# Performance work log

Hardware: AMD Instinct MI355X
Metric: run time of the kernel (lower is better)

## Reference

```python
import jax, jax.numpy as jnp
import numpy as np

B, N, C, H = 2, 2048, 768, 12
D = C // H
HID = 4 * C  # 3072
EPS = 1e-5
PAD = 128  # last PAD key positions are padded


def _layer_norm(x, w, b):
    m = jnp.mean(x, axis=-1, keepdims=True)
    v = jnp.var(x, axis=-1, keepdims=True)
    return (x - m) * jax.lax.rsqrt(v + EPS) * w + b


def setup_inputs() -> dict:
    key = jax.random.key(0)
    ks = jax.random.split(key, 12)
    s = 0.02
    inp = {
        'x': jax.random.normal(ks[0], (B, N, C), jnp.float32),
        # keys at positions >= N-PAD are padded (mask must have some True to be exercised)
        'padding_mask': jnp.broadcast_to(jnp.arange(N) >= N - PAD, (B, N)),
        'alibi_bias': jax.random.normal(ks[1], (B, H, N, N), jnp.float32) * 0.1,
        'qkv_w': jax.random.normal(ks[2], (3 * C, C), jnp.float32) * s,
        'qkv_b': jnp.zeros((3 * C,), jnp.float32),
        'proj_w': jax.random.normal(ks[3], (C, C), jnp.float32) * s,
        'proj_b': jnp.zeros((C,), jnp.float32),
        'norm1_w': jnp.ones((C,), jnp.float32),
        'norm1_b': jnp.zeros((C,), jnp.float32),
        'norm2_w': jnp.ones((C,), jnp.float32),
        'norm2_b': jnp.zeros((C,), jnp.float32),
        'fc1_w': jax.random.normal(ks[4], (HID, C), jnp.float32) * s,
        'fc1_b': jnp.zeros((HID,), jnp.float32),
        'fc2_w': jax.random.normal(ks[5], (C, HID), jnp.float32) * s,
        'fc2_b': jnp.zeros((C,), jnp.float32),
    }
    return inp


def _attention(x, padding_mask, alibi_bias, qkv_w, qkv_b, proj_w, proj_b):
    scale = D ** (-0.5)
    qkv = (x @ qkv_w.T + qkv_b).reshape(B, N, 3, H, D).transpose(2, 0, 3, 1, 4)
    q, k, v = qkv[0] * scale, qkv[1], qkv[2]  # [B,H,N,D]
    attn = jnp.einsum('bhnd,bhmd->bhnm', q, k)
    attn = attn + alibi_bias  # alibi covers all heads here
    attn = jnp.where(padding_mask[:, None, None, :], -jnp.inf, attn)
    attn = jax.nn.softmax(attn.astype(jnp.float32), axis=-1).astype(x.dtype)
    out = jnp.einsum('bhnm,bhmd->bhnd', attn, v)
    out = out.transpose(0, 2, 1, 3).reshape(B, N, C)
    return out @ proj_w.T + proj_b


def _mlp(x, fc1_w, fc1_b, fc2_w, fc2_b):
    h = jax.nn.gelu(x @ fc1_w.T + fc1_b, approximate=False)
    return h @ fc2_w.T + fc2_b


def reference(x, padding_mask, alibi_bias, qkv_w, qkv_b, proj_w, proj_b,
              norm1_w, norm1_b, norm2_w, norm2_b, fc1_w, fc1_b, fc2_w, fc2_b):
    # layer_norm_first=True, eval mode (dropouts/drop_path = identity)
    h = x + _attention(_layer_norm(x, norm1_w, norm1_b), padding_mask, alibi_bias,
                       qkv_w, qkv_b, proj_w, proj_b)
    # Faithful to source quirk: `r = x = self.mlp(self.norm2(x))` drops the residual,
    # so output = mlp_out + mlp_out and t = mlp_out.
    t = _mlp(_layer_norm(h, norm2_w, norm2_b), fc1_w, fc1_b, fc2_w, fc2_b)
    return (t + t, t)
```

## Files before the change

### kernel.cpp

```cpp
#include <hip/hip_runtime.h>
#include <cstdint>
#include <cstddef>

#define B_   2
#define N_   2048
#define C_   768
#define H_   12
#define D_   64
#define HID_ 3072
#define BH_  24
#define MM   4096

typedef __attribute__((ext_vector_type(8))) short s16x8;
typedef __attribute__((ext_vector_type(4))) short s16x4;
typedef __attribute__((ext_vector_type(4))) float f32x4;

__device__ __forceinline__ short f2bf(float f) {
  uint32_t u = __float_as_uint(f);
  u += 0x7fffu + ((u >> 16) & 1u);
  return (short)(u >> 16);
}

__device__ __forceinline__ void gl_lds16(const void* g, void* l) {
  __builtin_amdgcn_global_load_lds((const __attribute__((address_space(1))) void*)g,
                                   (__attribute__((address_space(3))) void*)l,
                                   16, 0, 0);
}

__device__ __forceinline__ float gelu_tanh(float v) {
  const float z  = 0.7978845608f * v * (1.0f + 0.044715f * v * v);
  const float e  = __expf(-2.0f * fabsf(z));
  const float th = copysignf((1.0f - e) / (1.0f + e), z);
  return 0.5f * v * (1.0f + th);
}

__global__ __launch_bounds__(256) void k_cvt4(
    const float* __restrict__ a, short* __restrict__ oa,
    const float* __restrict__ b, short* __restrict__ ob,
    const float* __restrict__ c, short* __restrict__ oc,
    const float* __restrict__ d, short* __restrict__ od) {
  const int blk = blockIdx.x;
  const float* in; short* out; int base;
  if (blk < 1728)      { in = a; out = oa; base = blk; }
  else if (blk < 2304) { in = b; out = ob; base = blk - 1728; }
  else if (blk < 4608) { in = c; out = oc; base = blk - 2304; }
  else                 { in = d; out = od; base = blk - 4608; }
  const int i = (base * 256 + threadIdx.x) * 4;
  float4 v = *(const float4*)(in + i);
  s16x4 o;
  o[0] = f2bf(v.x); o[1] = f2bf(v.y); o[2] = f2bf(v.z); o[3] = f2bf(v.w);
  *(s16x4*)(out + i) = o;
}

__global__ __launch_bounds__(256) void k_ln(const float* __restrict__ x,
                                            const float* __restrict__ w,
                                            const float* __restrict__ b,
                                            short* __restrict__ out) {
  const int row = blockIdx.x, t = threadIdx.x;
  const float* xr = x + (size_t)row * C_;
  float a0 = xr[t], a1 = xr[t + 256], a2 = xr[t + 512];
  float s = a0 + a1 + a2;
  float q = a0 * a0 + a1 * a1 + a2 * a2;
  #pragma unroll
  for (int off = 32; off >= 1; off >>= 1) {
    s += __shfl_xor(s, off);
    q += __shfl_xor(q, off);
  }
  __shared__ float ps[4], pq[4];
  if ((t & 63) == 0) { ps[t >> 6] = s; pq[t >> 6] = q; }
  __syncthreads();
  s = ps[0] + ps[1] + ps[2] + ps[3];
  q = pq[0] + pq[1] + pq[2] + pq[3];
  const float mean = s * (1.0f / C_);
  const float var  = q * (1.0f / C_) - mean * mean;
  const float rs   = rsqrtf(var + 1e-5f);
  short* orow = out + (size_t)row * C_;
  orow[t]       = f2bf((a0 - mean) * rs * w[t]       + b[t]);
  orow[t + 256] = f2bf((a1 - mean) * rs * w[t + 256] + b[t + 256]);
  orow[t + 512] = f2bf((a2 - mean) * rs * w[t + 512] + b[t + 512]);
}

__device__ __forceinline__ void gemm_core(const short* __restrict__ A,
                                          const short* __restrict__ Bw,
                                          int ldk, int kbeg, int kend,
                                          short* As, short* Bs,
                                          f32x4 acc[4][4]) {
  const int tid = threadIdx.x, lane = tid & 63, wid = tid >> 6;
  const int wm = wid & 1, wn = wid >> 1;
  const int l15 = lane & 15, quad = lane >> 4;
  const size_t bm = (size_t)blockIdx.x * 128, bn = (size_t)blockIdx.y * 128;
  #pragma unroll
  for (int mi = 0; mi < 4; ++mi)
    #pragma unroll
    for (int ni = 0; ni < 4; ++ni)
      acc[mi][ni] = (f32x4){0.f, 0.f, 0.f, 0.f};
  const int rrow = lane >> 2;
  const int rcol = (lane & 3) * 8;
  for (int k0 = kbeg; k0 < kend; k0 += 32) {
    #pragma unroll
    for (int i = 0; i < 2; ++i) {
      const int rg = wid * 2 + i;
      gl_lds16(A  + (bm + rg * 16 + rrow) * (size_t)ldk + k0 + rcol, As + rg * 512);
      gl_lds16(Bw + (bn + rg * 16 + rrow) * (size_t)ldk + k0 + rcol, Bs + rg * 512);
    }
    __syncthreads();
    s16x8 af[4], bf[4];
    #pragma unroll
    for (int mi = 0; mi < 4; ++mi)
      af[mi] = *(const s16x8*)(As + (wm * 64 + mi * 16 + l15) * 32 + quad * 8);
    #pragma unroll
    for (int ni = 0; ni < 4; ++ni)
      bf[ni] = *(const s16x8*)(Bs + (wn * 64 + ni * 16 + l15) * 32 + quad * 8);
    #pragma unroll
    for (int mi = 0; mi < 4; ++mi)
      #pragma unroll
      for (int ni = 0; ni < 4; ++ni)
        acc[mi][ni] = __builtin_amdgcn_mfma_f32_16x16x32_bf16(af[mi], bf[ni],
                                                              acc[mi][ni], 0, 0, 0);
    __syncthreads();
  }
}

__global__ __launch_bounds__(256) void k_gemm_qkv(const short* __restrict__ A,
    const short* __restrict__ W, const float* __restrict__ bias,
    short* __restrict__ qb, short* __restrict__ kb, short* __restrict__ vb) {
  __shared__ short As[4096], Bs[4096];
  f32x4 acc[4][4];
  gemm_core(A, W, C_, 0, C_, As, Bs, acc);
  const int lane = threadIdx.x & 63, wid = threadIdx.x >> 6;
  const int wm = wid & 1, wn = wid >> 1, quad = lane >> 4, l15 = lane & 15;
  const int m0 = blockIdx.x * 128 + wm * 64;
  const int n0 = blockIdx.y * 128 + wn * 64;
  #pragma unroll
  for (int ni = 0; ni < 4; ++ni) {
    const int n = n0 + ni * 16 + l15;
    const int s = n / C_, rem = n % C_;
    const int h = rem >> 6, d = rem & 63;
    short* dst = (s == 0) ? qb : (s == 1) ? kb : vb;
    const float scale = (s == 0) ? 0.125f : 1.0f;
    const float bv = bias[n];
    #pragma unroll
    for (int mi = 0; mi < 4; ++mi)
      #pragma unroll
      for (int r = 0; r < 4; ++r) {
        const int m = m0 + mi * 16 + quad * 4 + r;
        const int bb = m >> 11, pos = m & 2047;
        dst[(((size_t)bb * H_ + h) * N_ + pos) * D_ + d] =
            f2bf((acc[mi][ni][r] + bv) * scale);
      }
  }
}

__global__ __launch_bounds__(256) void k_trans_v(const short* __restrict__ v,
                                                 short* __restrict__ vt) {
  __shared__ short t[64][68];
  const int bh = blockIdx.y;
  const int p0 = blockIdx.x * 64;
  #pragma unroll
  for (int i = 0; i < 16; ++i) {
    const int idx = threadIdx.x + i * 256;
    const int r = idx >> 6, c = idx & 63;
    t[r][c] = v[((size_t)bh * N_ + p0 + r) * D_ + c];
  }
  __syncthreads();
  #pragma unroll
  for (int i = 0; i < 16; ++i) {
    const int idx = threadIdx.x + i * 256;
    const int r = idx >> 6, c = idx & 63;
    vt[((size_t)bh * D_ + r) * N_ + p0 + c] = t[c][r];
  }
}

__global__ __launch_bounds__(256) void k_attn(const short* __restrict__ qb,
    const short* __restrict__ kb, const short* __restrict__ vtb,
    const float* __restrict__ alibi, const int* __restrict__ mask,
    short* __restrict__ aout) {
  __shared__ short Ks[64 * 72], Vs[64 * 72];
  const int tid = threadIdx.x, lane = tid & 63, wid = tid >> 6;
  const int quad = lane >> 4, l15 = lane & 15;
  const int bh = blockIdx.y, bb = bh / H_, hh = bh % H_;
  const int qg = blockIdx.x * 64 + wid * 16 + l15;

  const short* qrow = qb + ((size_t)bh * N_ + qg) * D_;
  const s16x8 qf0 = *(const s16x8*)(qrow + quad * 8);
  const s16x8 qf1 = *(const s16x8*)(qrow + 32 + quad * 8);

  f32x4 oacc[4];
  #pragma unroll
  for (int i = 0; i < 4; ++i) oacc[i] = (f32x4){0.f, 0.f, 0.f, 0.f};
  float mrun = -1e30f, lrun = 0.f;

  const float* arow = alibi + ((size_t)bh * N_ + qg) * N_;
  const int* mrow = mask + bb * N_;

  for (int jt = 0; jt < N_; jt += 64) {
    int4 mk[4];
    int anyvalid = 0;
    #pragma unroll
    for (int ji = 0; ji < 4; ++ji) {
      mk[ji] = *(const int4*)(mrow + jt + ji * 16 + quad * 4);
      if (!(mk[ji].x && mk[ji].y && mk[ji].z && mk[ji].w)) anyvalid = 1;
    }
    if (!__any(anyvalid)) continue;

    #pragma unroll
    for (int c = 0; c < 2; ++c) {
      const int idx = tid + c * 256;
      const int row = idx >> 3, col = (idx & 7) * 8;
      *(int4*)(&Ks[row * 72 + col]) =
          *(const int4*)(kb + ((size_t)bh * N_ + jt + row) * D_ + col);
      *(int4*)(&Vs[row * 72 + col]) =
          *(const int4*)(vtb + ((size_t)bh * D_ + row) * N_ + jt + col);
    }
    __syncthreads();

    f32x4 s[4];
    #pragma unroll
    for (int ji = 0; ji < 4; ++ji) {
      const s16x8 ka = *(const s16x8*)(&Ks[(ji * 16 + l15) * 72 + quad * 8]);
      const s16x8 kc = *(const s16x8*)(&Ks[(ji * 16 + l15) * 72 + 32 + quad * 8]);
      f32x4 z = (f32x4){0.f, 0.f, 0.f, 0.f};
      z = __builtin_amdgcn_mfma_f32_16x16x32_bf16(ka, qf0, z, 0, 0, 0);
      s[ji] = __builtin_amdgcn_mfma_f32_16x16x32_bf16(kc, qf1, z, 0, 0, 0);
    }

    float p[4][4];
    float mt = -1e30f;
    #pragma unroll
    for (int ji = 0; ji < 4; ++ji) {
      const float4 al = *(const float4*)(arow + jt + ji * 16 + quad * 4);
      float v0 = s[ji][0] + al.x; if (mk[ji].x) v0 = -1e30f;
      float v1 = s[ji][1] + al.y; if (mk[ji].y) v1 = -1e30f;
      float v2 = s[ji][2] + al.z; if (mk[ji].z) v2 = -1e30f;
      float v3 = s[ji][3] + al.w; if (mk[ji].w) v3 = -1e30f;
      p[ji][0] = v0; p[ji][1] = v1; p[ji][2] = v2; p[ji][3] = v3;
      mt = fmaxf(mt, fmaxf(fmaxf(v0, v1), fmaxf(v2, v3)));
    }
    mt = fmaxf(mt, __shfl_xor(mt, 16));
    mt = fmaxf(mt, __shfl_xor(mt, 32));
    const float mnew = fmaxf(mrun, mt);
    const float scl = __expf(mrun - mnew);
    float psum = 0.f;
    s16x4 pf[4];
    #pragma unroll
    for (int ji = 0; ji < 4; ++ji)
      #pragma unroll
      for (int r = 0; r < 4; ++r) {
        const float e = __expf(p[ji][r] - mnew);
        psum += e;
        pf[ji][r] = f2bf(e);
      }
    psum += __shfl_xor(psum, 16);
    psum += __shfl_xor(psum, 32);
    lrun = lrun * scl + psum;
    mrun = mnew;
    #pragma unroll
    for (int i = 0; i < 4; ++i) oacc[i] *= scl;

    #pragma unroll
    for (int ji = 0; ji < 4; ++ji)
      #pragma unroll
      for (int ni = 0; ni < 4; ++ni) {
        const s16x4 vf = *(const s16x4*)(&Vs[(ni * 16 + l15) * 72 + ji * 16 + quad * 4]);
        oacc[ni] = __builtin_amdgcn_mfma_f32_16x16x16bf16_1k(vf, pf[ji],
                                                             oacc[ni], 0, 0, 0);
      }
    __syncthreads();
  }

  const float inv = 1.0f / lrun;
  short* orow = aout + ((size_t)bb * N_ + qg) * C_ + hh * D_;
  #pragma unroll
  for (int ni = 0; ni < 4; ++ni)
    #pragma unroll
    for (int r = 0; r < 4; ++r)
      orow[ni * 16 + quad * 4 + r] = f2bf(oacc[ni][r] * inv);
}

__global__ __launch_bounds__(256) void k_gemm_projs(const short* __restrict__ A,
    const short* __restrict__ W, float* __restrict__ part) {
  __shared__ short As[4096], Bs[4096];
  f32x4 acc[4][4];
  const int z = blockIdx.z;
  gemm_core(A, W, C_, z * 384, z * 384 + 384, As, Bs, acc);
  const int lane = threadIdx.x & 63, wid = threadIdx.x >> 6;
  const int wm = wid & 1, wn = wid >> 1, quad = lane >> 4, l15 = lane & 15;
  const int m0 = blockIdx.x * 128 + wm * 64;
  const int n0 = blockIdx.y * 128 + wn * 64;
  float* pz = part + (size_t)z * MM * C_;
  #pragma unroll
  for (int ni = 0; ni < 4; ++ni) {
    const int n = n0 + ni * 16 + l15;
    #pragma unroll
    for (int mi = 0; mi < 4; ++mi)
      #pragma unroll
      for (int r = 0; r < 4; ++r) {
        const int m = m0 + mi * 16 + quad * 4 + r;
        pz[(size_t)m * C_ + n] = acc[mi][ni][r];
      }
  }
}

__global__ __launch_bounds__(256) void k_proj_red(const float* __restrict__ p,
    const float* __restrict__ bias, const float* __restrict__ xres,
    float* __restrict__ hout) {
  const int i = (blockIdx.x * 256 + threadIdx.x) * 4;
  const float4 s0 = *(const float4*)(p + i);
  const float4 s1 = *(const float4*)(p + (size_t)MM * C_ + i);
  const float4 bv = *(const float4*)(bias + (i % C_));
  const float4 xr = *(const float4*)(xres + i);
  float4 o;
  o.x = s0.x + s1.x + bv.x + xr.x;
  o.y = s0.y + s1.y + bv.y + xr.y;
  o.z = s0.z + s1.z + bv.z + xr.z;
  o.w = s0.w + s1.w + bv.w + xr.w;
  *(float4*)(hout + i) = o;
}

__global__ __launch_bounds__(256) void k_gemm_fc1(const short* __restrict__ A,
    const short* __restrict__ W, const float* __restrict__ bias,
    short* __restrict__ hid) {
  __shared__ short As[4096], Bs[4096];
  f32x4 acc[4][4];
  gemm_core(A, W, C_, 0, C_, As, Bs, acc);
  const int lane = threadIdx.x & 63, wid = threadIdx.x >> 6;
  const int wm = wid & 1, wn = wid >> 1, quad = lane >> 4, l15 = lane & 15;
  const int m0 = blockIdx.x * 128 + wm * 64;
  const int n0 = blockIdx.y * 128 + wn * 64;
  #pragma unroll
  for (int ni = 0; ni < 4; ++ni) {
    const int n = n0 + ni * 16 + l15;
    const float bv = bias[n];
    #pragma unroll
    for (int mi = 0; mi < 4; ++mi)
      #pragma unroll
      for (int r = 0; r < 4; ++r) {
        const int m = m0 + mi * 16 + quad * 4 + r;
        hid[(size_t)m * HID_ + n] = f2bf(gelu_tanh(acc[mi][ni][r] + bv));
      }
  }
}

__global__ __launch_bounds__(256) void k_gemm_fc2s(const short* __restrict__ A,
    const short* __restrict__ W, float* __restrict__ part) {
  __shared__ short As[4096], Bs[4096];
  f32x4 acc[4][4];
  const int z = blockIdx.z;
  gemm_core(A, W, HID_, z * 768, z * 768 + 768, As, Bs, acc);
  const int lane = threadIdx.x & 63, wid = threadIdx.x >> 6;
  const int wm = wid & 1, wn = wid >> 1, quad = lane >> 4, l15 = lane & 15;
  const int m0 = blockIdx.x * 128 + wm * 64;
  const int n0 = blockIdx.y * 128 + wn * 64;
  float* pz = part + (size_t)z * MM * C_;
  #pragma unroll
  for (int ni = 0; ni < 4; ++ni) {
    const int n = n0 + ni * 16 + l15;
    #pragma unroll
    for (int mi = 0; mi < 4; ++mi)
      #pragma unroll
      for (int r = 0; r < 4; ++r) {
        const int m = m0 + mi * 16 + quad * 4 + r;
        pz[(size_t)m * C_ + n] = acc[mi][ni][r];
      }
  }
}

__global__ __launch_bounds__(256) void k_fc2_red(const float* __restrict__ p,
    const float* __restrict__ bias, float* __restrict__ out) {
  const int i = (blockIdx.x * 256 + threadIdx.x) * 4;
  const float4 s0 = *(const float4*)(p + i);
  const float4 s1 = *(const float4*)(p + (size_t)MM * C_ + i);
  const float4 s2 = *(const float4*)(p + (size_t)2 * MM * C_ + i);
  const float4 s3 = *(const float4*)(p + (size_t)3 * MM * C_ + i);
  const float4 bv = *(const float4*)(bias + (i % C_));
  float4 t, t2;
  t.x = s0.x + s1.x + s2.x + s3.x + bv.x;  t2.x = t.x + t.x;
  t.y = s0.y + s1.y + s2.y + s3.y + bv.y;  t2.y = t.y + t.y;
  t.z = s0.z + s1.z + s2.z + s3.z + bv.z;  t2.z = t.z + t.z;
  t.w = s0.w + s1.w + s2.w + s3.w + bv.w;  t2.w = t.w + t.w;
  *(float4*)(out + i) = t2;
  *(float4*)(out + (size_t)MM * C_ + i) = t;
}

extern "C" void kernel_launch(void* const* d_in, const int* in_sizes, int n_in,
                              void* d_out, int out_size, void* d_ws, size_t ws_size,
                              hipStream_t stream) {
  (void)in_sizes; (void)n_in; (void)out_size; (void)ws_size;
  const float* x      = (const float*)d_in[0];
  const int*   mask   = (const int*)  d_in[1];
  const float* alibi  = (const float*)d_in[2];
  const float* qkv_w  = (const float*)d_in[3];
  const float* qkv_b  = (const float*)d_in[4];
  const float* proj_w = (const float*)d_in[5];
  const float* proj_b = (const float*)d_in[6];
  const float* n1w    = (const float*)d_in[7];
  const float* n1b    = (const float*)d_in[8];
  const float* n2w    = (const float*)d_in[9];
  const float* n2b    = (const float*)d_in[10];
  const float* fc1_w  = (const float*)d_in[11];
  const float* fc1_b  = (const float*)d_in[12];
  const float* fc2_w  = (const float*)d_in[13];
  const float* fc2_b  = (const float*)d_in[14];
  float* out = (float*)d_out;

  char* ws = (char*)d_ws;
  size_t off = 0;
  auto alloc = [&](size_t bytes) -> void* {
    void* p = ws + off;
    off += (bytes + 255) & ~(size_t)255;
    return p;
  };
  short* wq   = (short*)alloc((size_t)3 * C_ * C_ * 2);
  short* wp   = (short*)alloc((size_t)C_ * C_ * 2);
  short* wf1  = (short*)alloc((size_t)HID_ * C_ * 2);
  short* wf2  = (short*)alloc((size_t)C_ * HID_ * 2);
  short* xln  = (short*)alloc((size_t)MM * C_ * 2);
  short* qb   = (short*)alloc((size_t)BH_ * N_ * D_ * 2);
  short* kb   = (short*)alloc((size_t)BH_ * N_ * D_ * 2);
  short* vb   = (short*)alloc((size_t)BH_ * N_ * D_ * 2);
  short* vtb  = (short*)alloc((size_t)BH_ * D_ * N_ * 2);
  float* h    = (float*)alloc((size_t)MM * C_ * 4);
  short* hid  = (short*)alloc((size_t)MM * HID_ * 2);
  float* ppj  = (float*)alloc((size_t)2 * MM * C_ * 4);
  float* pf2  = (float*)alloc((size_t)4 * MM * C_ * 4);
  short* hln  = xln;
  short* aout = vb;

  k_cvt4<<<6912, 256, 0, stream>>>(qkv_w, wq, proj_w, wp, fc1_w, wf1, fc2_w, wf2);

  k_ln<<<MM, 256, 0, stream>>>(x, n1w, n1b, xln);
  k_gemm_qkv<<<dim3(MM / 128, 3 * C_ / 128), 256, 0, stream>>>(xln, wq, qkv_b,
                                                               qb, kb, vb);
  k_trans_v<<<dim3(N_ / 64, BH_), 256, 0, stream>>>(vb, vtb);
  k_attn<<<dim3(N_ / 64, BH_), 256, 0, stream>>>(qb, kb, vtb, alibi, mask, aout);
  k_gemm_projs<<<dim3(MM / 128, C_ / 128, 2), 256, 0, stream>>>(aout, wp, ppj);
  k_proj_red<<<MM * C_ / 1024, 256, 0, stream>>>(ppj, proj_b, x, h);
  k_ln<<<MM, 256, 0, stream>>>(h, n2w, n2b, hln);
  k_gemm_fc1<<<dim3(MM / 128, HID_ / 128), 256, 0, stream>>>(hln, wf1, fc1_b, hid);
  k_gemm_fc2s<<<dim3(MM / 128, C_ / 128, 4), 256, 0, stream>>>(hid, wf2, pf2);
  k_fc2_red<<<MM * C_ / 1024, 256, 0, stream>>>(pf2, fc2_b, out);
}
```

Measured before the change: 749.4 us.

## Fuse LN with weight casts, fuse proj reduction into LN2, widen GEMM/attention tiles

Merges the weight bf16 conversion and first layernorm into one launch, and folds the projection split-K reduction and residual add into the second layernorm so the fp32 h buffer is never written. The shared GEMM core now stages a K-step of 64 per barrier instead of 32, halving the synchronisations. Attention processes 128-key tiles loaded through direct global-to-LDS copies, with the padding mask precomputed once per block as an additive LDS vector and per-tile skip flags. This trades extra LDS per block, which may lower occupancy, for fewer launches, fewer barriers and less memory traffic.

```diff
diff --git a/kernel.cpp b/kernel.cpp
--- a/kernel.cpp
+++ b/kernel.cpp
@@ -34,50 +34,50 @@
   return 0.5f * v * (1.0f + th);
 }
 
-__global__ __launch_bounds__(256) void k_cvt4(
+__global__ __launch_bounds__(256) void k_pre(const float* __restrict__ x,
+    const float* __restrict__ n1w, const float* __restrict__ n1b,
+    short* __restrict__ xln,
     const float* __restrict__ a, short* __restrict__ oa,
     const float* __restrict__ b, short* __restrict__ ob,
     const float* __restrict__ c, short* __restrict__ oc,
     const float* __restrict__ d, short* __restrict__ od) {
-  const int blk = blockIdx.x;
-  const float* in; short* out; int base;
-  if (blk < 1728)      { in = a; out = oa; base = blk; }
-  else if (blk < 2304) { in = b; out = ob; base = blk - 1728; }
-  else if (blk < 4608) { in = c; out = oc; base = blk - 2304; }
-  else                 { in = d; out = od; base = blk - 4608; }
-  const int i = (base * 256 + threadIdx.x) * 4;
-  float4 v = *(const float4*)(in + i);
-  s16x4 o;
-  o[0] = f2bf(v.x); o[1] = f2bf(v.y); o[2] = f2bf(v.z); o[3] = f2bf(v.w);
-  *(s16x4*)(out + i) = o;
-}
-
-__global__ __launch_bounds__(256) void k_ln(const float* __restrict__ x,
-                                            const float* __restrict__ w,
-                                            const float* __restrict__ b,
-                                            short* __restrict__ out) {
-  const int row = blockIdx.x, t = threadIdx.x;
-  const float* xr = x + (size_t)row * C_;
-  float a0 = xr[t], a1 = xr[t + 256], a2 = xr[t + 512];
-  float s = a0 + a1 + a2;
-  float q = a0 * a0 + a1 * a1 + a2 * a2;
-  #pragma unroll
-  for (int off = 32; off >= 1; off >>= 1) {
-    s += __shfl_xor(s, off);
-    q += __shfl_xor(q, off);
-  }
-  __shared__ float ps[4], pq[4];
-  if ((t & 63) == 0) { ps[t >> 6] = s; pq[t >> 6] = q; }
-  __syncthreads();
-  s = ps[0] + ps[1] + ps[2] + ps[3];
-  q = pq[0] + pq[1] + pq[2] + pq[3];
-  const float mean = s * (1.0f / C_);
-  const float var  = q * (1.0f / C_) - mean * mean;
-  const float rs   = rsqrtf(var + 1e-5f);
-  short* orow = out + (size_t)row * C_;
-  orow[t]       = f2bf((a0 - mean) * rs * w[t]       + b[t]);
-  orow[t + 256] = f2bf((a1 - mean) * rs * w[t + 256] + b[t + 256]);
-  orow[t + 512] = f2bf((a2 - mean) * rs * w[t + 512] + b[t + 512]);
+  const int t = threadIdx.x;
+  if (blockIdx.x < MM) {
+    const int row = blockIdx.x;
+    const float* xr = x + (size_t)row * C_;
+    float a0 = xr[t], a1 = xr[t + 256], a2 = xr[t + 512];
+    float s = a0 + a1 + a2;
+    float q = a0 * a0 + a1 * a1 + a2 * a2;
+    #pragma unroll
+    for (int off = 32; off >= 1; off >>= 1) {
+      s += __shfl_xor(s, off);
+      q += __shfl_xor(q, off);
+    }
+    __shared__ float ps[4], pq[4];
+    if ((t & 63) == 0) { ps[t >> 6] = s; pq[t >> 6] = q; }
+    __syncthreads();
+    s = ps[0] + ps[1] + ps[2] + ps[3];
+    q = pq[0] + pq[1] + pq[2] + pq[3];
+    const float mean = s * (1.0f / C_);
+    const float var  = q * (1.0f / C_) - mean * mean;
+    const float rs   = rsqrtf(var + 1e-5f);
+    short* orow = xln + (size_t)row * C_;
+    orow[t]       = f2bf((a0 - mean) * rs * n1w[t]       + n1b[t]);
+    orow[t + 256] = f2bf((a1 - mean) * rs * n1w[t + 256] + n1b[t + 256]);
+    orow[t + 512] = f2bf((a2 - mean) * rs * n1w[t + 512] + n1b[t + 512]);
+  } else {
+    const int blk = blockIdx.x - MM;
+    const float* in; short* out; int base;
+    if (blk < 1728)      { in = a; out = oa; base = blk; }
+    else if (blk < 2304) { in = b; out = ob; base = blk - 1728; }
+    else if (blk < 4608) { in = c; out = oc; base = blk - 2304; }
+    else                 { in = d; out = od; base = blk - 4608; }
+    const int i = (base * 256 + t) * 4;
+    float4 v = *(const float4*)(in + i);
+    s16x4 o;
+    o[0] = f2bf(v.x); o[1] = f2bf(v.y); o[2] = f2bf(v.z); o[3] = f2bf(v.w);
+    *(s16x4*)(out + i) = o;
+  }
 }
 
 __device__ __forceinline__ void gemm_core(const short* __restrict__ A,
@@ -94,29 +94,36 @@
     #pragma unroll
     for (int ni = 0; ni < 4; ++ni)
       acc[mi][ni] = (f32x4){0.f, 0.f, 0.f, 0.f};
-  const int rrow = lane >> 2;
-  const int rcol = (lane & 3) * 8;
-  for (int k0 = kbeg; k0 < kend; k0 += 32) {
-    #pragma unroll
-    for (int i = 0; i < 2; ++i) {
-      const int rg = wid * 2 + i;
-      gl_lds16(A  + (bm + rg * 16 + rrow) * (size_t)ldk + k0 + rcol, As + rg * 512);
-      gl_lds16(Bw + (bn + rg * 16 + rrow) * (size_t)ldk + k0 + rcol, Bs + rg * 512);
-    }
+  const int r4 = lane >> 2;
+  const int c4 = lane & 3;
+  for (int k0 = kbeg; k0 < kend; k0 += 64) {
+    #pragma unroll
+    for (int p = 0; p < 2; ++p)
+      #pragma unroll
+      for (int c = 0; c < 2; ++c) {
+        const int g = c * 4 + wid;
+        gl_lds16(A  + (bm + g * 16 + r4) * (size_t)ldk + k0 + p * 32 + c4 * 8,
+                 As + p * 4096 + g * 512);
+        gl_lds16(Bw + (bn + g * 16 + r4) * (size_t)ldk + k0 + p * 32 + c4 * 8,
+                 Bs + p * 4096 + g * 512);
+      }
     __syncthreads();
-    s16x8 af[4], bf[4];
-    #pragma unroll
-    for (int mi = 0; mi < 4; ++mi)
-      af[mi] = *(const s16x8*)(As + (wm * 64 + mi * 16 + l15) * 32 + quad * 8);
-    #pragma unroll
-    for (int ni = 0; ni < 4; ++ni)
-      bf[ni] = *(const s16x8*)(Bs + (wn * 64 + ni * 16 + l15) * 32 + quad * 8);
-    #pragma unroll
-    for (int mi = 0; mi < 4; ++mi)
+    #pragma unroll
+    for (int h = 0; h < 2; ++h) {
+      s16x8 af[4], bf[4];
+      #pragma unroll
+      for (int mi = 0; mi < 4; ++mi)
+        af[mi] = *(const s16x8*)(As + h * 4096 + (wm * 64 + mi * 16 + l15) * 32 + quad * 8);
       #pragma unroll
       for (int ni = 0; ni < 4; ++ni)
-        acc[mi][ni] = __builtin_amdgcn_mfma_f32_16x16x32_bf16(af[mi], bf[ni],
-                                                              acc[mi][ni], 0, 0, 0);
+        bf[ni] = *(const s16x8*)(Bs + h * 4096 + (wn * 64 + ni * 16 + l15) * 32 + quad * 8);
+      #pragma unroll
+      for (int mi = 0; mi < 4; ++mi)
+        #pragma unroll
+        for (int ni = 0; ni < 4; ++ni)
+          acc[mi][ni] = __builtin_amdgcn_mfma_f32_16x16x32_bf16(af[mi], bf[ni],
+                                                                acc[mi][ni], 0, 0, 0);
+    }
     __syncthreads();
   }
 }
@@ -124,7 +131,7 @@
 __global__ __launch_bounds__(256) void k_gemm_qkv(const short* __restrict__ A,
     const short* __restrict__ W, const float* __restrict__ bias,
     short* __restrict__ qb, short* __restrict__ kb, short* __restrict__ vb) {
-  __shared__ short As[4096], Bs[4096];
+  __shared__ short As[8192], Bs[8192];
   f32x4 acc[4][4];
   gemm_core(A, W, C_, 0, C_, As, Bs, acc);
   const int lane = threadIdx.x & 63, wid = threadIdx.x >> 6;
@@ -175,11 +182,29 @@
     const short* __restrict__ kb, const short* __restrict__ vtb,
     const float* __restrict__ alibi, const int* __restrict__ mask,
     short* __restrict__ aout) {
-  __shared__ short Ks[64 * 72], Vs[64 * 72];
+  __shared__ short Ks[8192];
+  __shared__ short Vs[8192];
+  __shared__ float Madd[N_];
+  __shared__ int   Tflag[16];
   const int tid = threadIdx.x, lane = tid & 63, wid = tid >> 6;
   const int quad = lane >> 4, l15 = lane & 15;
+  const int r4 = lane >> 2, c4 = lane & 3;
   const int bh = blockIdx.y, bb = bh / H_, hh = bh % H_;
   const int qg = blockIdx.x * 64 + wid * 16 + l15;
+
+  if (tid < 16) Tflag[tid] = 0;
+  __syncthreads();
+  {
+    const int j0 = tid * 8;
+    int anyv = 0;
+    #pragma unroll
+    for (int i = 0; i < 8; ++i) {
+      const int mv = mask[bb * N_ + j0 + i];
+      Madd[j0 + i] = mv ? -1e30f : 0.0f;
+      anyv |= (mv == 0);
+    }
+    if (anyv) atomicOr(&Tflag[j0 >> 7], 1);
+  }
 
   const short* qrow = qb + ((size_t)bh * N_ + qg) * D_;
   const s16x8 qf0 = *(const s16x8*)(qrow + quad * 8);
@@ -189,51 +214,47 @@
   #pragma unroll
   for (int i = 0; i < 4; ++i) oacc[i] = (f32x4){0.f, 0.f, 0.f, 0.f};
   float mrun = -1e30f, lrun = 0.f;
-
   const float* arow = alibi + ((size_t)bh * N_ + qg) * N_;
-  const int* mrow = mask + bb * N_;
-
-  for (int jt = 0; jt < N_; jt += 64) {
-    int4 mk[4];
-    int anyvalid = 0;
-    #pragma unroll
-    for (int ji = 0; ji < 4; ++ji) {
-      mk[ji] = *(const int4*)(mrow + jt + ji * 16 + quad * 4);
-      if (!(mk[ji].x && mk[ji].y && mk[ji].z && mk[ji].w)) anyvalid = 1;
-    }
-    if (!__any(anyvalid)) continue;
-
-    #pragma unroll
-    for (int c = 0; c < 2; ++c) {
-      const int idx = tid + c * 256;
-      const int row = idx >> 3, col = (idx & 7) * 8;
-      *(int4*)(&Ks[row * 72 + col]) =
-          *(const int4*)(kb + ((size_t)bh * N_ + jt + row) * D_ + col);
-      *(int4*)(&Vs[row * 72 + col]) =
-          *(const int4*)(vtb + ((size_t)bh * D_ + row) * N_ + jt + col);
-    }
+  __syncthreads();
+
+  for (int t = 0; t < 16; ++t) {
+    if (!Tflag[t]) continue;
+    const int jt = t * 128;
+    #pragma unroll
+    for (int p = 0; p < 2; ++p)
+      #pragma unroll
+      for (int c = 0; c < 2; ++c) {
+        const int g = c * 4 + wid;
+        gl_lds16(kb + ((size_t)bh * N_ + jt + g * 16 + r4) * D_ + p * 32 + c4 * 8,
+                 Ks + p * 4096 + g * 512);
+      }
+    #pragma unroll
+    for (int p = 0; p < 4; ++p)
+      gl_lds16(vtb + ((size_t)bh * D_ + wid * 16 + r4) * N_ + jt + p * 32 + c4 * 8,
+               Vs + p * 2048 + wid * 512);
     __syncthreads();
 
-    f32x4 s[4];
-    #pragma unroll
-    for (int ji = 0; ji < 4; ++ji) {
-      const s16x8 ka = *(const s16x8*)(&Ks[(ji * 16 + l15) * 72 + quad * 8]);
-      const s16x8 kc = *(const s16x8*)(&Ks[(ji * 16 + l15) * 72 + 32 + quad * 8]);
+    f32x4 s[8];
+    #pragma unroll
+    for (int ji = 0; ji < 8; ++ji) {
+      const s16x8 ka = *(const s16x8*)(Ks + (ji * 16 + l15) * 32 + quad * 8);
+      const s16x8 kc = *(const s16x8*)(Ks + 4096 + (ji * 16 + l15) * 32 + quad * 8);
       f32x4 z = (f32x4){0.f, 0.f, 0.f, 0.f};
       z = __builtin_amdgcn_mfma_f32_16x16x32_bf16(ka, qf0, z, 0, 0, 0);
       s[ji] = __builtin_amdgcn_mfma_f32_16x16x32_bf16(kc, qf1, z, 0, 0, 0);
     }
 
-    float p[4][4];
+    float p_[8][4];
     float mt = -1e30f;
     #pragma unroll
-    for (int ji = 0; ji < 4; ++ji) {
+    for (int ji = 0; ji < 8; ++ji) {
       const float4 al = *(const float4*)(arow + jt + ji * 16 + quad * 4);
-      float v0 = s[ji][0] + al.x; if (mk[ji].x) v0 = -1e30f;
-      float v1 = s[ji][1] + al.y; if (mk[ji].y) v1 = -1e30f;
-      float v2 = s[ji][2] + al.z; if (mk[ji].z) v2 = -1e30f;
-      float v3 = s[ji][3] + al.w; if (mk[ji].w) v3 = -1e30f;
-      p[ji][0] = v0; p[ji][1] = v1; p[ji][2] = v2; p[ji][3] = v3;
+      const float4 md = *(const float4*)(&Madd[jt + ji * 16 + quad * 4]);
+      const float v0 = s[ji][0] + al.x + md.x;
+      const float v1 = s[ji][1] + al.y + md.y;
+      const float v2 = s[ji][2] + al.z + md.z;
+      const float v3 = s[ji][3] + al.w + md.w;
+      p_[ji][0] = v0; p_[ji][1] = v1; p_[ji][2] = v2; p_[ji][3] = v3;
       mt = fmaxf(mt, fmaxf(fmaxf(v0, v1), fmaxf(v2, v3)));
     }
     mt = fmaxf(mt, __shfl_xor(mt, 16));
@@ -241,12 +262,12 @@
     const float mnew = fmaxf(mrun, mt);
     const float scl = __expf(mrun - mnew);
     float psum = 0.f;
-    s16x4 pf[4];
-    #pragma unroll
-    for (int ji = 0; ji < 4; ++ji)
+    s16x4 pf[8];
+    #pragma unroll
+    for (int ji = 0; ji < 8; ++ji)
       #pragma unroll
       for (int r = 0; r < 4; ++r) {
-        const float e = __expf(p[ji][r] - mnew);
+        const float e = __expf(p_[ji][r] - mnew);
         psum += e;
         pf[ji][r] = f2bf(e);
       }
@@ -258,13 +279,15 @@
     for (int i = 0; i < 4; ++i) oacc[i] *= scl;
 
     #pragma unroll
-    for (int ji = 0; ji < 4; ++ji)
+    for (int jj = 0; jj < 8; ++jj) {
+      const int pnl = jj >> 1, jw = (jj & 1) * 16 + quad * 4;
       #pragma unroll
       for (int ni = 0; ni < 4; ++ni) {
-        const s16x4 vf = *(const s16x4*)(&Vs[(ni * 16 + l15) * 72 + ji * 16 + quad * 4]);
-        oacc[ni] = __builtin_amdgcn_mfma_f32_16x16x16bf16_1k(vf, pf[ji],
+        const s16x4 vf = *(const s16x4*)(Vs + pnl * 2048 + (ni * 16 + l15) * 32 + jw);
+        oacc[ni] = __builtin_amdgcn_mfma_f32_16x16x16bf16_1k(vf, pf[jj],
                                                              oacc[ni], 0, 0, 0);
       }
+    }
     __syncthreads();
   }
 
@@ -279,7 +302,7 @@
 
 __global__ __launch_bounds__(256) void k_gemm_projs(const short* __restrict__ A,
     const short* __restrict__ W, float* __restrict__ part) {
-  __shared__ short As[4096], Bs[4096];
+  __shared__ short As[8192], Bs[8192];
   f32x4 acc[4][4];
   const int z = blockIdx.z;
   gemm_core(A, W, C_, z * 384, z * 384 + 384, As, Bs, acc);
@@ -301,26 +324,43 @@
   }
 }
 
-__global__ __launch_bounds__(256) void k_proj_red(const float* __restrict__ p,
+__global__ __launch_bounds__(256) void k_ln2p(const float* __restrict__ p,
     const float* __restrict__ bias, const float* __restrict__ xres,
-    float* __restrict__ hout) {
-  const int i = (blockIdx.x * 256 + threadIdx.x) * 4;
-  const float4 s0 = *(const float4*)(p + i);
-  const float4 s1 = *(const float4*)(p + (size_t)MM * C_ + i);
-  const float4 bv = *(const float4*)(bias + (i % C_));
-  const float4 xr = *(const float4*)(xres + i);
-  float4 o;
-  o.x = s0.x + s1.x + bv.x + xr.x;
-  o.y = s0.y + s1.y + bv.y + xr.y;
-  o.z = s0.z + s1.z + bv.z + xr.z;
-  o.w = s0.w + s1.w + bv.w + xr.w;
-  *(float4*)(hout + i) = o;
+    const float* __restrict__ w, const float* __restrict__ b,
+    short* __restrict__ out) {
+  const int row = blockIdx.x, t = threadIdx.x;
+  const size_t base = (size_t)row * C_;
+  float a0 = p[base + t]       + p[(size_t)MM * C_ + base + t]
+           + bias[t]           + xres[base + t];
+  float a1 = p[base + t + 256] + p[(size_t)MM * C_ + base + t + 256]
+           + bias[t + 256]     + xres[base + t + 256];
+  float a2 = p[base + t + 512] + p[(size_t)MM * C_ + base + t + 512]
+           + bias[t + 512]     + xres[base + t + 512];
+  float s = a0 + a1 + a2;
+  float q = a0 * a0 + a1 * a1 + a2 * a2;
+  #pragma unroll
+  for (int off = 32; off >= 1; off >>= 1) {
+    s += __shfl_xor(s, off);
+    q += __shfl_xor(q, off);
+  }
+  __shared__ float ps[4], pq[4];
+  if ((t & 63) == 0) { ps[t >> 6] = s; pq[t >> 6] = q; }
+  __syncthreads();
+  s = ps[0] + ps[1] + ps[2] + ps[3];
+  q = pq[0] + pq[1] + pq[2] + pq[3];
+  const float mean = s * (1.0f / C_);
+  const float var  = q * (1.0f / C_) - mean * mean;
+  const float rs   = rsqrtf(var + 1e-5f);
+  short* orow = out + base;
+  orow[t]       = f2bf((a0 - mean) * rs * w[t]       + b[t]);
+  orow[t + 256] = f2bf((a1 - mean) * rs * w[t + 256] + b[t + 256]);
+  orow[t + 512] = f2bf((a2 - mean) * rs * w[t + 512] + b[t + 512]);
 }
 
 __global__ __launch_bounds__(256) void k_gemm_fc1(const short* __restrict__ A,
     const short* __restrict__ W, const float* __restrict__ bias,
     short* __restrict__ hid) {
-  __shared__ short As[4096], Bs[4096];
+  __shared__ short As[8192], Bs[8192];
   f32x4 acc[4][4];
   gemm_core(A, W, C_, 0, C_, As, Bs, acc);
   const int lane = threadIdx.x & 63, wid = threadIdx.x >> 6;
@@ -343,7 +383,7 @@
 
 __global__ __launch_bounds__(256) void k_gemm_fc2s(const short* __restrict__ A,
     const short* __restrict__ W, float* __restrict__ part) {
-  __shared__ short As[4096], Bs[4096];
+  __shared__ short As[8192], Bs[8192];
   f32x4 acc[4][4];
   const int z = blockIdx.z;
   gemm_core(A, W, HID_, z * 768, z * 768 + 768, As, Bs, acc);
@@ -419,23 +459,21 @@
   short* kb   = (short*)alloc((size_t)BH_ * N_ * D_ * 2);
   short* vb   = (short*)alloc((size_t)BH_ * N_ * D_ * 2);
   short* vtb  = (short*)alloc((size_t)BH_ * D_ * N_ * 2);
-  float* h    = (float*)alloc((size_t)MM * C_ * 4);
   short* hid  = (short*)alloc((size_t)MM * HID_ * 2);
   float* ppj  = (float*)alloc((size_t)2 * MM * C_ * 4);
   float* pf2  = (float*)alloc((size_t)4 * MM * C_ * 4);
   short* hln  = xln;
   short* aout = vb;
 
-  k_cvt4<<<6912, 256, 0, stream>>>(qkv_w, wq, proj_w, wp, fc1_w, wf1, fc2_w, wf2);
-
-  k_ln<<<MM, 256, 0, stream>>>(x, n1w, n1b, xln);
+  k_pre<<<MM + 6912, 256, 0, stream>>>(x, n1w, n1b, xln,
+                                       qkv_w, wq, proj_w, wp,
+                                       fc1_w, wf1, fc2_w, wf2);
   k_gemm_qkv<<<dim3(MM / 128, 3 * C_ / 128), 256, 0, stream>>>(xln, wq, qkv_b,
                                                                qb, kb, vb);
   k_trans_v<<<dim3(N_ / 64, BH_), 256, 0, stream>>>(vb, vtb);
   k_attn<<<dim3(N_ / 64, BH_), 256, 0, stream>>>(qb, kb, vtb, alibi, mask, aout);
   k_gemm_projs<<<dim3(MM / 128, C_ / 128, 2), 256, 0, stream>>>(aout, wp, ppj);
-  k_proj_red<<<MM * C_ / 1024, 256, 0, stream>>>(ppj, proj_b, x, h);
-  k_ln<<<MM, 256, 0, stream>>>(h, n2w, n2b, hln);
+  k_ln2p<<<MM, 256, 0, stream>>>(ppj, proj_b, x, n2w, n2b, hln);
   k_gemm_fc1<<<dim3(MM / 128, HID_ / 128), 256, 0, stream>>>(hln, wf1, fc1_b, hid);
   k_gemm_fc2s<<<dim3(MM / 128, C_ / 128, 4), 256, 0, stream>>>(hid, wf2, pf2);
   k_fc2_red<<<MM * C_ / 1024, 256, 0, stream>>>(pf2, fc2_b, out);
```

Result: slower. 781.8 us (+4.3%).
